# Optimization experiments

Hardware: AMD Instinct MI355X
Metric: run time of the kernel (lower is better)

## Reference

```python
import jax, jax.numpy as jnp
import numpy as np

HEADS, DHEAD = 8, 32
INNER = HEADS * DHEAD  # 256


def _conv3x3(x, w, b):
    y = jax.lax.conv_general_dilated(x, w, (1, 1), ((1, 1), (1, 1)),
                                     dimension_numbers=('NCHW', 'OIHW', 'NCHW'))
    return y + b[None, :, None, None]


def _conv1x1(x, w, b):
    return jnp.einsum('oc,bchw->bohw', w, x) + b[None, :, None, None]


def setup_inputs() -> dict:
    key = jax.random.key(0)
    ks = jax.random.split(key, 16)
    s = 0.02
    return {
        'x': jax.random.normal(ks[0], (2, 256, 48, 48), jnp.float32),
        'luma': jax.random.uniform(ks[1], (2, 1, 48, 48), jnp.float32),
        'w_qkv': jax.random.normal(ks[2], (768, 256), jnp.float32) * s,
        'b_qkv': jax.random.normal(ks[3], (768,), jnp.float32) * s,
        'w_proj': jax.random.normal(ks[4], (256, 256), jnp.float32) * s,
        'b_proj': jax.random.normal(ks[5], (256,), jnp.float32) * s,
        'w_c1': jax.random.normal(ks[6], (128, 1, 3, 3), jnp.float32) * s,
        'b_c1': jax.random.normal(ks[7], (128,), jnp.float32) * s,
        'w_c2': jax.random.normal(ks[8], (128, 128, 3, 3), jnp.float32) * s,
        'b_c2': jax.random.normal(ks[9], (128,), jnp.float32) * s,
        'w_g': jax.random.normal(ks[10], (256, 128), jnp.float32) * s,
        'b_g': jax.random.normal(ks[11], (256,), jnp.float32) * s,
        'w_bt': jax.random.normal(ks[12], (256, 128), jnp.float32) * s,
        'b_bt': jax.random.normal(ks[13], (256,), jnp.float32) * s,
        'alpha': jax.random.normal(ks[14], (), jnp.float32) * 0.1,
    }


def reference(x, luma, w_qkv, b_qkv, w_proj, b_proj, w_c1, b_c1, w_c2, b_c2,
              w_g, b_g, w_bt, b_bt, alpha):
    B, C, H, W = x.shape
    N = H * W
    scale = DHEAD ** -0.5

    def to_heads(t):  # [B, h*d, H, W] -> [B, h, N, d]
        return t.reshape(B, HEADS, DHEAD, N).transpose(0, 1, 3, 2)

    qkv = _conv1x1(x, w_qkv, b_qkv)
    q = to_heads(qkv[:, 0 * INNER:1 * INNER])
    k = to_heads(qkv[:, 1 * INNER:2 * INNER])
    v = to_heads(qkv[:, 2 * INNER:3 * INNER])

    # luma conditioning net
    h = jax.nn.relu(_conv3x3(luma, w_c1, b_c1))
    h = jax.nn.relu(_conv3x3(h, w_c2, b_c2))
    gamma = to_heads(_conv1x1(h, w_g, b_g))
    beta = to_heads(_conv1x1(h, w_bt, b_bt))
    q = gamma * q + beta
    k = gamma * k + beta
    v = gamma * v + beta

    # luminance bias: avg_pool2d(3, stride=1, pad=1, count_include_pad=True)
    invL = 1.0 - luma
    invL = jax.lax.reduce_window(invL, 0.0, jax.lax.add, (1, 1, 3, 3), (1, 1, 1, 1),
                                 ((0, 0), (0, 0), (1, 1), (1, 1))) / 9.0
    invL = invL.reshape(B, N)
    invL = invL - invL.mean(axis=-1, keepdims=True)
    q = q + alpha * invL[:, None, :, None]

    attn = jax.nn.softmax(jnp.einsum('bhid,bhjd->bhij', q, k) * scale, axis=-1)
    out = jnp.einsum('bhij,bhjd->bhid', attn, v)
    out = out.transpose(0, 1, 3, 2).reshape(B, INNER, H, W)
    return _conv1x1(out, w_proj, b_proj)
```

## Files before the change

kernel.cpp:

```cpp
#include <hip/hip_runtime.h>
#include <hip/hip_bf16.h>
#include <math.h>
#include <string.h>

#define NB 2
#define NN 2304
#define NHEADS 8
#define DH 32
#define AW 8
#define KPW 288

typedef __attribute__((ext_vector_type(8))) short v8s;
typedef __attribute__((ext_vector_type(4))) float v4f;

__device__ inline unsigned short f2b(float f) {
    unsigned u = __builtin_bit_cast(unsigned, f);
    unsigned r = u + 0x7FFFu + ((u >> 16) & 1u);
    return (unsigned short)(r >> 16);
}
__device__ inline float b2f(short s) {
    unsigned u = ((unsigned)(unsigned short)s) << 16;
    return __builtin_bit_cast(float, u);
}
__device__ inline unsigned pk2(float a, float b) {
    __hip_bfloat162 h = __float22bfloat162_rn(make_float2(a, b));
    unsigned r;
    memcpy(&r, &h, sizeof(r));
    return r;
}
__device__ inline float blo(unsigned u) { return __builtin_bit_cast(float, u << 16); }
__device__ inline float bhi(unsigned u) { return __builtin_bit_cast(float, u & 0xffff0000u); }

__global__ void k_front(const float* __restrict__ x, short* __restrict__ xt,
                        const float* __restrict__ luma, float* __restrict__ invl,
                        const float* __restrict__ wc1, const float* __restrict__ bc1,
                        short* __restrict__ h1p,
                        const float* __restrict__ wc2, const float* __restrict__ wqkv,
                        const float* __restrict__ wg, const float* __restrict__ wbt,
                        const float* __restrict__ wproj,
                        short* __restrict__ tc2b, short* __restrict__ wqkvb,
                        short* __restrict__ wgb, short* __restrict__ wbtb,
                        short* __restrict__ wprojb, float* __restrict__ vsum) {
    __shared__ unsigned short lds[64 * 66];
    __shared__ float red[256];
    int blk = blockIdx.x;
    const int XT_END = NB * 144;
    const int INVL_END = XT_END + NB;
    const int CONV1_END = INVL_END + NB * 1250;
    if (blk >= CONV1_END) {
        int i = (blk - CONV1_END) * 256 + threadIdx.x;
        if (i < 16 * DH) vsum[i] = 0.f;
        if (i < 9 * 128 * 128) {
            int s = i / (128 * 128);
            int rem = i % (128 * 128);
            int o = rem / 128, ic = rem % 128;
            tc2b[i] = (short)f2b(wc2[(o * 128 + ic) * 9 + s]);
        }
        if (i < 768 * 256) wqkvb[i] = (short)f2b(wqkv[i]);
        if (i < 256 * 128) { wgb[i] = (short)f2b(wg[i]); wbtb[i] = (short)f2b(wbt[i]); }
        if (i < 256 * 256) wprojb[i] = (short)f2b(wproj[i]);
        return;
    }
    if (blk >= INVL_END) {
        int cb = blk - INVL_END;
        int c = threadIdx.x & 127;
        int p = (cb % 1250) * 2 + (threadIdx.x >> 7);
        int b = cb / 1250;
        int py = p / 50, px = p % 50;
        float val = 0.f;
        if (py >= 1 && py <= 48 && px >= 1 && px <= 48) {
            int y = py - 1, xx0 = px - 1;
            const float* lb = luma + b * NN;
            float acc = bc1[c];
#pragma unroll
            for (int ky = 0; ky < 3; ++ky) {
                int yy = y + ky - 1;
                if (yy < 0 || yy >= 48) continue;
#pragma unroll
                for (int kx = 0; kx < 3; ++kx) {
                    int xx = xx0 + kx - 1;
                    if (xx < 0 || xx >= 48) continue;
                    acc += wc1[c * 9 + ky * 3 + kx] * lb[yy * 48 + xx];
                }
            }
            val = fmaxf(acc, 0.f);
        }
        h1p[((size_t)b * 2500 + p) * 128 + c] = (short)f2b(val);
        return;
    }
    if (blk >= XT_END) {
        int b = blk - XT_END;
        const float* lb = luma + b * NN;
        float pooled[9];
        float local = 0.f;
#pragma unroll
        for (int it = 0; it < 9; ++it) {
            int n = it * 256 + threadIdx.x;
            int y = n / 48, xx0 = n % 48;
            float s = 0.f;
            for (int ky = 0; ky < 3; ++ky) {
                int yy = y + ky - 1;
                if (yy < 0 || yy >= 48) continue;
                for (int kx = 0; kx < 3; ++kx) {
                    int xx = xx0 + kx - 1;
                    if (xx < 0 || xx >= 48) continue;
                    s += 1.f - lb[yy * 48 + xx];
                }
            }
            s *= (1.f / 9.f);
            pooled[it] = s;
            local += s;
        }
        red[threadIdx.x] = local;
        __syncthreads();
        for (int off = 128; off > 0; off >>= 1) {
            if (threadIdx.x < off) red[threadIdx.x] += red[threadIdx.x + off];
            __syncthreads();
        }
        float mean = red[0] * (1.f / NN);
#pragma unroll
        for (int it = 0; it < 9; ++it) {
            int n = it * 256 + threadIdx.x;
            invl[b * NN + n] = pooled[it] - mean;
        }
        return;
    }
    int nt = blk % 36, ct = (blk / 36) % 4, b = blk / 144;
    int n0 = nt * 64, c0 = ct * 64;
    int nc = threadIdx.x & 63, cr = threadIdx.x >> 6;
#pragma unroll
    for (int i = 0; i < 16; ++i) {
        int cs = i * 4 + cr;
        float v = x[((size_t)b * 256 + c0 + cs) * NN + n0 + nc];
        lds[nc * 66 + cs] = f2b(v);
    }
    __syncthreads();
    int cc = threadIdx.x & 31, nr = threadIdx.x >> 5;
    unsigned* xt2 = (unsigned*)xt;
#pragma unroll
    for (int j = 0; j < 8; ++j) {
        int ns = j * 8 + nr;
        unsigned w = *(unsigned*)&lds[ns * 66 + 2 * cc];
        xt2[(((size_t)b * NN + n0 + ns) * 256 + c0) / 2 + cc] = w;
    }
}

__global__ __launch_bounds__(64) void k_conv2m(const short* __restrict__ h1p,
                                               const short* __restrict__ tc2b,
                                               const float* __restrict__ bc2,
                                               short* __restrict__ h2t) {
    int lane = threadIdx.x, l15 = lane & 15, g = lane >> 4;
    int blk = blockIdx.x;
    int ntg = blk % 36, ot = (blk / 36) % 8, b = blk / (36 * 8);
    int p0[4], na[4];
#pragma unroll
    for (int j = 0; j < 4; ++j) {
        int nt = ntg * 4 + j;
        int y = nt / 3, xx = (nt % 3) * 16;
        p0[j] = (y + 1) * 50 + xx + 1;
        na[j] = y * 48 + xx + l15;
    }
    const short* hb = h1p + (size_t)b * 2500 * 128;

    v4f acc[4] = {{0.f,0.f,0.f,0.f},{0.f,0.f,0.f,0.f},{0.f,0.f,0.f,0.f},{0.f,0.f,0.f,0.f}};
#pragma unroll
    for (int s = 0; s < 9; ++s) {
        int dp = (s / 3 - 1) * 50 + (s % 3 - 1);
#pragma unroll
        for (int kk = 0; kk < 4; ++kk) {
            v8s A = *(const v8s*)(tc2b + ((size_t)(s * 128 + ot * 16 + l15)) * 128 + kk * 32 + 8 * g);
#pragma unroll
            for (int j = 0; j < 4; ++j) {
                v8s B = *(const v8s*)(hb + (size_t)(p0[j] + dp + l15) * 128 + kk * 32 + 8 * g);
                acc[j] = __builtin_amdgcn_mfma_f32_16x16x32_bf16(A, B, acc[j], 0, 0, 0);
            }
        }
    }
    v4f bias = *(const v4f*)&bc2[ot * 16 + 4 * g];
#pragma unroll
    for (int j = 0; j < 4; ++j) {
        uint2 w;
        w.x = pk2(fmaxf(acc[j][0] + bias[0], 0.f), fmaxf(acc[j][1] + bias[1], 0.f));
        w.y = pk2(fmaxf(acc[j][2] + bias[2], 0.f), fmaxf(acc[j][3] + bias[3], 0.f));
        *(uint2*)&h2t[((size_t)b * NN + na[j]) * 128 + ot * 16 + 4 * g] = w;
    }
}

__global__ __launch_bounds__(64) void k_gbm(const short* __restrict__ h2t,
                                            const short* __restrict__ wgb,
                                            const short* __restrict__ wbtb,
                                            const float* __restrict__ bg,
                                            const float* __restrict__ bbt,
                                            short* __restrict__ gtb, short* __restrict__ bttb) {
    int lane = threadIdx.x, l15 = lane & 15, g = lane >> 4;
    int blk = blockIdx.x;
    int ntg = blk % 36, ot = (blk / 36) % 16, b = blk / (36 * 16);
    int n0 = ntg * 64;
    const short* hb = h2t + (size_t)b * NN * 128;

    v4f ga[4] = {{0.f,0.f,0.f,0.f},{0.f,0.f,0.f,0.f},{0.f,0.f,0.f,0.f},{0.f,0.f,0.f,0.f}};
    v4f ta[4] = {{0.f,0.f,0.f,0.f},{0.f,0.f,0.f,0.f},{0.f,0.f,0.f,0.f},{0.f,0.f,0.f,0.f}};
#pragma unroll
    for (int kk = 0; kk < 4; ++kk) {
        v8s Ag = *(const v8s*)(wgb + (size_t)(ot * 16 + l15) * 128 + kk * 32 + 8 * g);
        v8s At = *(const v8s*)(wbtb + (size_t)(ot * 16 + l15) * 128 + kk * 32 + 8 * g);
#pragma unroll
        for (int j = 0; j < 4; ++j) {
            v8s B = *(const v8s*)(hb + (size_t)(n0 + j * 16 + l15) * 128 + kk * 32 + 8 * g);
            ga[j] = __builtin_amdgcn_mfma_f32_16x16x32_bf16(Ag, B, ga[j], 0, 0, 0);
            ta[j] = __builtin_amdgcn_mfma_f32_16x16x32_bf16(At, B, ta[j], 0, 0, 0);
        }
    }
    v4f bgv = *(const v4f*)&bg[ot * 16 + 4 * g];
    v4f bbv = *(const v4f*)&bbt[ot * 16 + 4 * g];
#pragma unroll
    for (int j = 0; j < 4; ++j) {
        size_t o = ((size_t)b * NN + n0 + j * 16 + l15) * 256 + ot * 16 + 4 * g;
        uint2 w;
        w.x = pk2(ga[j][0] + bgv[0], ga[j][1] + bgv[1]);
        w.y = pk2(ga[j][2] + bgv[2], ga[j][3] + bgv[3]);
        *(uint2*)&gtb[o] = w;
        w.x = pk2(ta[j][0] + bbv[0], ta[j][1] + bbv[1]);
        w.y = pk2(ta[j][2] + bbv[2], ta[j][3] + bbv[3]);
        *(uint2*)&bttb[o] = w;
    }
}

__global__ __launch_bounds__(64) void k_qkvm(const short* __restrict__ xt,
                                             const short* __restrict__ wqkvb,
                                             const float* __restrict__ bqkv,
                                             const short* __restrict__ gtb,
                                             const short* __restrict__ bttb,
                                             const float* __restrict__ invl,
                                             const float* __restrict__ alpha_p,
                                             short* __restrict__ qb, short* __restrict__ kb,
                                             short* __restrict__ vtb, float* __restrict__ vsum) {
    __shared__ unsigned short vlds[64][36];
    int lane = threadIdx.x, l15 = lane & 15, g = lane >> 4;
    int blk = blockIdx.x;
    int ntg = blk % 36, otg = (blk / 36) % 24, b = blk / (36 * 24);
    int n0 = ntg * 64;
    const short* xb = xt + (size_t)b * NN * 256;

    v4f acc[2][4];
#pragma unroll
    for (int oa = 0; oa < 2; ++oa)
#pragma unroll
        for (int j = 0; j < 4; ++j) acc[oa][j] = (v4f){0.f, 0.f, 0.f, 0.f};
#pragma unroll
    for (int kk = 0; kk < 8; ++kk) {
        v8s A0 = *(const v8s*)(wqkvb + (size_t)(otg * 32 + l15) * 256 + kk * 32 + 8 * g);
        v8s A1 = *(const v8s*)(wqkvb + (size_t)(otg * 32 + 16 + l15) * 256 + kk * 32 + 8 * g);
#pragma unroll
        for (int j = 0; j < 4; ++j) {
            v8s B = *(const v8s*)(xb + (size_t)(n0 + j * 16 + l15) * 256 + kk * 32 + 8 * g);
            acc[0][j] = __builtin_amdgcn_mfma_f32_16x16x32_bf16(A0, B, acc[0][j], 0, 0, 0);
            acc[1][j] = __builtin_amdgcn_mfma_f32_16x16x32_bf16(A1, B, acc[1][j], 0, 0, 0);
        }
    }
    const float scale = 0.25503486f;
    float alpha = *alpha_p;
    int which = (otg * 32) >> 8;
#pragma unroll
    for (int oa = 0; oa < 2; ++oa) {
        int ocb = otg * 32 + oa * 16;
        int cbase = (ocb & 255) + 4 * g;
        int h = cbase >> 5, dbase = cbase & 31;
        v4f bias = *(const v4f*)&bqkv[ocb + 4 * g];
        short* dst = (which == 0) ? qb : kb;
#pragma unroll
        for (int j = 0; j < 4; ++j) {
            int n = n0 + j * 16 + l15;
            v4f a = acc[oa][j];
            uint2 gg = *(const uint2*)&gtb[((size_t)b * NN + n) * 256 + cbase];
            uint2 tt = *(const uint2*)&bttb[((size_t)b * NN + n) * 256 + cbase];
            float iv = (which == 0) ? alpha * invl[b * NN + n] : 0.f;
            float v0 = blo(gg.x) * (a[0] + bias[0]) + blo(tt.x);
            float v1 = bhi(gg.x) * (a[1] + bias[1]) + bhi(tt.x);
            float v2 = blo(gg.y) * (a[2] + bias[2]) + blo(tt.y);
            float v3 = bhi(gg.y) * (a[3] + bias[3]) + bhi(tt.y);
            if (which == 0) {
                v0 = (v0 + iv) * scale; v1 = (v1 + iv) * scale;
                v2 = (v2 + iv) * scale; v3 = (v3 + iv) * scale;
            }
            uint2 wv;
            wv.x = pk2(v0, v1);
            wv.y = pk2(v2, v3);
            if (which == 2) {
                *(uint2*)&vlds[j * 16 + l15][oa * 16 + 4 * g] = wv;
            } else {
                *(uint2*)&dst[(((size_t)b * NHEADS + h) * NN + n) * DH + dbase] = wv;
            }
        }
    }
    if (which == 2) {
        __syncthreads();
        int bh = b * NHEADS + (otg - 16);
        int kb0 = ntg * 2;
        int kp = lane & 31, dh = lane >> 5;
        unsigned* vtb2 = (unsigned*)vtb;
#pragma unroll
        for (int dd = 0; dd < 16; ++dd) {
            int d = dh * 16 + dd;
            unsigned lo = vlds[2 * kp][d];
            unsigned hi = vlds[2 * kp + 1][d];
            vtb2[(((size_t)bh * 72 + kb0 + (kp >> 4)) * 32 + d) * 16 + (kp & 15)] = lo | (hi << 16);
        }
        if (lane < 32) {
            int d = lane;
            float s = 0.f;
            for (int ns = 0; ns < 64; ++ns) s += b2f((short)vlds[ns][d]);
            atomicAdd(&vsum[bh * DH + d], s);
        }
    }
}

__global__ __launch_bounds__(512) void k_attn2(const short* __restrict__ qb,
                                               const short* __restrict__ kbuf,
                                               const short* __restrict__ vtb,
                                               const float* __restrict__ vsum,
                                               short* __restrict__ aotb) {
    __shared__ short plds[AW][64 * 40];
    __shared__ short acch[AW][64][36];
    __shared__ float ps_lds[AW][64];
    int tid = threadIdx.x;
    int w = tid >> 6, lane = tid & 63;
    int l15 = lane & 15, g = lane >> 4;
    int blk = blockIdx.x;
    int logical = (blk & 7) * 72 + (blk >> 3);
    int qt = logical % 36, bh = logical / 36;
    int qbase = qt * 64;

    const short* qp = qb + ((size_t)bh * NN + qbase) * DH;
    const short* kp = kbuf + ((size_t)bh * NN + w * KPW) * DH;
    const short* vp = vtb + ((size_t)bh * 72 + w * (KPW / 32)) * 1024;

    v8s q0 = *(const v8s*)(qp + l15 * DH + 8 * g);
    v8s q1 = *(const v8s*)(qp + (16 + l15) * DH + 8 * g);
    v8s q2 = *(const v8s*)(qp + (32 + l15) * DH + 8 * g);
    v8s q3 = *(const v8s*)(qp + (48 + l15) * DH + 8 * g);

    const short one_b = (short)0x3F80;
    const v8s ones = {one_b, one_b, one_b, one_b, one_b, one_b, one_b, one_b};

    v4f acc[2][4];
#pragma unroll
    for (int dt = 0; dt < 2; ++dt)
#pragma unroll
        for (int qf = 0; qf < 4; ++qf) acc[dt][qf] = (v4f){0.f, 0.f, 0.f, 0.f};
    v4f ps[4] = {{0.f,0.f,0.f,0.f},{0.f,0.f,0.f,0.f},{0.f,0.f,0.f,0.f},{0.f,0.f,0.f,0.f}};
    short* pw = plds[w];

    for (int it = 0; it < KPW / 32; ++it) {
        const short* kpi = kp + it * 32 * DH;
        v8s ka0 = *(const v8s*)(kpi + l15 * DH + 8 * g);
        v8s ka1 = *(const v8s*)(kpi + (16 + l15) * DH + 8 * g);
        v4f s00 = __builtin_amdgcn_mfma_f32_16x16x32_bf16(ka0, q0, (v4f){0.f,0.f,0.f,0.f}, 0, 0, 0);
        v4f s01 = __builtin_amdgcn_mfma_f32_16x16x32_bf16(ka0, q1, (v4f){0.f,0.f,0.f,0.f}, 0, 0, 0);
        v4f s02 = __builtin_amdgcn_mfma_f32_16x16x32_bf16(ka0, q2, (v4f){0.f,0.f,0.f,0.f}, 0, 0, 0);
        v4f s03 = __builtin_amdgcn_mfma_f32_16x16x32_bf16(ka0, q3, (v4f){0.f,0.f,0.f,0.f}, 0, 0, 0);
        v4f s10 = __builtin_amdgcn_mfma_f32_16x16x32_bf16(ka1, q0, (v4f){0.f,0.f,0.f,0.f}, 0, 0, 0);
        v4f s11 = __builtin_amdgcn_mfma_f32_16x16x32_bf16(ka1, q1, (v4f){0.f,0.f,0.f,0.f}, 0, 0, 0);
        v4f s12 = __builtin_amdgcn_mfma_f32_16x16x32_bf16(ka1, q2, (v4f){0.f,0.f,0.f,0.f}, 0, 0, 0);
        v4f s13 = __builtin_amdgcn_mfma_f32_16x16x32_bf16(ka1, q3, (v4f){0.f,0.f,0.f,0.f}, 0, 0, 0);

#define DOFRAG(S, QF, KT)                                                        \
        {                                                                        \
            float p0 = __builtin_amdgcn_exp2f((S)[0]) - 1.f;                     \
            float p1 = __builtin_amdgcn_exp2f((S)[1]) - 1.f;                     \
            float p2 = __builtin_amdgcn_exp2f((S)[2]) - 1.f;                     \
            float p3 = __builtin_amdgcn_exp2f((S)[3]) - 1.f;                     \
            uint2 wv;                                                            \
            wv.x = pk2(p0, p1);                                                  \
            wv.y = pk2(p2, p3);                                                  \
            *(uint2*)((char*)pw + ((QF) * 16 + l15) * 80 + ((KT) * 16 + 4 * g) * 2) = wv; \
        }
        DOFRAG(s00, 0, 0)
        DOFRAG(s01, 1, 0)
        DOFRAG(s02, 2, 0)
        DOFRAG(s03, 3, 0)
        DOFRAG(s10, 0, 1)
        DOFRAG(s11, 1, 1)
        DOFRAG(s12, 2, 1)
        DOFRAG(s13, 3, 1)
#undef DOFRAG
        v8s pa0 = *(v8s*)((char*)pw + l15 * 80 + 16 * g);
        v8s pa1 = *(v8s*)((char*)pw + (16 + l15) * 80 + 16 * g);
        v8s pa2 = *(v8s*)((char*)pw + (32 + l15) * 80 + 16 * g);
        v8s pa3 = *(v8s*)((char*)pw + (48 + l15) * 80 + 16 * g);
        const short* vpi = vp + it * 1024;
        v8s vb0 = *(const v8s*)(vpi + l15 * 32 + 8 * g);
        v8s vb1 = *(const v8s*)(vpi + (16 + l15) * 32 + 8 * g);
        __builtin_amdgcn_s_setprio(1);
        acc[0][0] = __builtin_amdgcn_mfma_f32_16x16x32_bf16(pa0, vb0, acc[0][0], 0, 0, 0);
        acc[1][0] = __builtin_amdgcn_mfma_f32_16x16x32_bf16(pa0, vb1, acc[1][0], 0, 0, 0);
        acc[0][1] = __builtin_amdgcn_mfma_f32_16x16x32_bf16(pa1, vb0, acc[0][1], 0, 0, 0);
        acc[1][1] = __builtin_amdgcn_mfma_f32_16x16x32_bf16(pa1, vb1, acc[1][1], 0, 0, 0);
        acc[0][2] = __builtin_amdgcn_mfma_f32_16x16x32_bf16(pa2, vb0, acc[0][2], 0, 0, 0);
        acc[1][2] = __builtin_amdgcn_mfma_f32_16x16x32_bf16(pa2, vb1, acc[1][2], 0, 0, 0);
        acc[0][3] = __builtin_amdgcn_mfma_f32_16x16x32_bf16(pa3, vb0, acc[0][3], 0, 0, 0);
        acc[1][3] = __builtin_amdgcn_mfma_f32_16x16x32_bf16(pa3, vb1, acc[1][3], 0, 0, 0);
        ps[0] = __builtin_amdgcn_mfma_f32_16x16x32_bf16(pa0, ones, ps[0], 0, 0, 0);
        ps[1] = __builtin_amdgcn_mfma_f32_16x16x32_bf16(pa1, ones, ps[1], 0, 0, 0);
        ps[2] = __builtin_amdgcn_mfma_f32_16x16x32_bf16(pa2, ones, ps[2], 0, 0, 0);
        ps[3] = __builtin_amdgcn_mfma_f32_16x16x32_bf16(pa3, ones, ps[3], 0, 0, 0);
        __builtin_amdgcn_s_setprio(0);
    }

    if (l15 == 0) {
#pragma unroll
        for (int qf = 0; qf < 4; ++qf)
#pragma unroll
            for (int r = 0; r < 4; ++r)
                ps_lds[w][qf * 16 + 4 * g + r] = ps[qf][r];
    }
#pragma unroll
    for (int qf = 0; qf < 4; ++qf)
#pragma unroll
        for (int r = 0; r < 4; ++r) {
            acch[w][qf * 16 + 4 * g + r][l15]      = (short)f2b(acc[0][qf][r]);
            acch[w][qf * 16 + 4 * g + r][16 + l15] = (short)f2b(acc[1][qf][r]);
        }
    __syncthreads();

    int q = tid >> 3, d0 = (tid & 7) * 4;
    float L = (float)NN;
    float a0 = 0.f, a1 = 0.f, a2 = 0.f, a3 = 0.f;
#pragma unroll
    for (int wv = 0; wv < AW; ++wv) {
        L += ps_lds[wv][q];
        const short* row = &acch[wv][q][d0];
        a0 += b2f(row[0]); a1 += b2f(row[1]); a2 += b2f(row[2]); a3 += b2f(row[3]);
    }
    const float* vs = vsum + bh * DH + d0;
    float rl = 1.f / L;
    uint2 o;
    o.x = pk2((a0 + vs[0]) * rl, (a1 + vs[1]) * rl);
    o.y = pk2((a2 + vs[2]) * rl, (a3 + vs[3]) * rl);
    int b = bh >> 3, h = bh & 7;
    *(uint2*)&aotb[((size_t)b * NN + qbase + q) * 256 + h * DH + d0] = o;
}

__global__ __launch_bounds__(64) void k_projm(const short* __restrict__ aotb,
                                              const short* __restrict__ wprojb,
                                              const float* __restrict__ bproj,
                                              float* __restrict__ out) {
    int lane = threadIdx.x, l15 = lane & 15, g = lane >> 4;
    int blk = blockIdx.x;
    int ntg = blk % 36, otg = (blk / 36) % 8, b = blk / (36 * 8);
    int n0 = ntg * 64;
    const short* ab = aotb + (size_t)b * NN * 256;

    v4f acc[2][4];
#pragma unroll
    for (int oa = 0; oa < 2; ++oa)
#pragma unroll
        for (int j = 0; j < 4; ++j) acc[oa][j] = (v4f){0.f, 0.f, 0.f, 0.f};
#pragma unroll
    for (int kk = 0; kk < 8; ++kk) {
        v8s A0 = *(const v8s*)(wprojb + (size_t)(otg * 32 + l15) * 256 + kk * 32 + 8 * g);
        v8s A1 = *(const v8s*)(wprojb + (size_t)(otg * 32 + 16 + l15) * 256 + kk * 32 + 8 * g);
#pragma unroll
        for (int j = 0; j < 4; ++j) {
            v8s B = *(const v8s*)(ab + (size_t)(n0 + j * 16 + l15) * 256 + kk * 32 + 8 * g);
            acc[0][j] = __builtin_amdgcn_mfma_f32_16x16x32_bf16(A0, B, acc[0][j], 0, 0, 0);
            acc[1][j] = __builtin_amdgcn_mfma_f32_16x16x32_bf16(A1, B, acc[1][j], 0, 0, 0);
        }
    }
#pragma unroll
    for (int oa = 0; oa < 2; ++oa) {
        v4f bias = *(const v4f*)&bproj[otg * 32 + oa * 16 + 4 * g];
#pragma unroll
        for (int j = 0; j < 4; ++j) {
#pragma unroll
            for (int r = 0; r < 4; ++r) {
                int o = otg * 32 + oa * 16 + 4 * g + r;
                out[((size_t)b * 256 + o) * NN + n0 + j * 16 + l15] = acc[oa][j][r] + bias[r];
            }
        }
    }
}

extern "C" void kernel_launch(void* const* d_in, const int* in_sizes, int n_in,
                              void* d_out, int out_size, void* d_ws, size_t ws_size,
                              hipStream_t stream) {
    const float* x     = (const float*)d_in[0];
    const float* luma  = (const float*)d_in[1];
    const float* wqkv  = (const float*)d_in[2];
    const float* bqkv  = (const float*)d_in[3];
    const float* wproj = (const float*)d_in[4];
    const float* bproj = (const float*)d_in[5];
    const float* wc1   = (const float*)d_in[6];
    const float* bc1   = (const float*)d_in[7];
    const float* wc2   = (const float*)d_in[8];
    const float* bc2   = (const float*)d_in[9];
    const float* wg    = (const float*)d_in[10];
    const float* bg    = (const float*)d_in[11];
    const float* wbt   = (const float*)d_in[12];
    const float* bbt   = (const float*)d_in[13];
    const float* alpha = (const float*)d_in[14];
    float* out = (float*)d_out;

    float* ws = (float*)d_ws;
    size_t off = 0;
    short* tc2b = (short*)(ws + off);  off += 9 * 128 * 128 / 2;
    short* wqkvb = (short*)(ws + off); off += 768 * 256 / 2;
    short* wgb = (short*)(ws + off);   off += 256 * 128 / 2;
    short* wbtb = (short*)(ws + off);  off += 256 * 128 / 2;
    short* wprojb = (short*)(ws + off); off += 256 * 256 / 2;
    short* h1p = (short*)(ws + off);   off += NB * 2500 * 128 / 2;
    short* xt = (short*)(ws + off);    off += NB * NN * 256 / 2;
    short* h2t = (short*)(ws + off);   off += NB * NN * 128 / 2;
    short* gtb = (short*)(ws + off);   off += NB * NN * 256 / 2;
    short* bttb = (short*)(ws + off);  off += NB * NN * 256 / 2;
    float* invl = ws + off;            off += NB * NN;
    short* qbb = (short*)(ws + off);   off += 16 * NN * DH / 2;
    short* kbb = (short*)(ws + off);   off += 16 * NN * DH / 2;
    short* vtb = (short*)(ws + off);   off += 16 * NN * DH / 2;
    float* vsum = ws + off;            off += 16 * DH;
    short* aotb = (short*)(ws + off);  off += NB * NN * 256 / 2;
    (void)ws_size; (void)in_sizes; (void)n_in; (void)out_size;

    int front_grid = NB * 144 + NB + NB * 1250 + 768;
    k_front<<<front_grid, 256, 0, stream>>>(x, xt, luma, invl, wc1, bc1, h1p,
                                            wc2, wqkv, wg, wbt, wproj,
                                            tc2b, wqkvb, wgb, wbtb, wprojb, vsum);
    k_conv2m<<<NB * 8 * 36, 64, 0, stream>>>(h1p, tc2b, bc2, h2t);
    k_gbm<<<NB * 16 * 36, 64, 0, stream>>>(h2t, wgb, wbtb, bg, bbt, gtb, bttb);
    k_qkvm<<<NB * 24 * 36, 64, 0, stream>>>(xt, wqkvb, bqkv, gtb, bttb, invl, alpha,
                                            qbb, kbb, vtb, vsum);
    k_attn2<<<576, 512, 0, stream>>>(qbb, kbb, vtb, vsum, aotb);
    k_projm<<<NB * 8 * 36, 64, 0, stream>>>(aotb, wprojb, bproj, out);
}
```

Baseline: 96.11 us.

## Use 32x32x16 MFMA in attention with register-resident P and smaller query tiles

Switches the attention kernel from 16x16x32 to 32x32x16 bf16 MFMA. K rows are loaded in a permuted order so the score accumulator layout already matches the A-operand layout for the PV product. This drops the per-iteration LDS round trip for the probability tile. The query tile shrinks from 64 to 32, which doubles the grid to 1152 blocks and halves the per-wave work, while each block still repeats the K/V loads.

```diff
diff --git a/kernel.cpp b/kernel.cpp
--- a/kernel.cpp
+++ b/kernel.cpp
@@ -12,6 +12,7 @@
 
 typedef __attribute__((ext_vector_type(8))) short v8s;
 typedef __attribute__((ext_vector_type(4))) float v4f;
+typedef __attribute__((ext_vector_type(16))) float v16f;
 
 __device__ inline unsigned short f2b(float f) {
     unsigned u = __builtin_bit_cast(unsigned, f);
@@ -320,125 +321,92 @@
                                                const short* __restrict__ vtb,
                                                const float* __restrict__ vsum,
                                                short* __restrict__ aotb) {
-    __shared__ short plds[AW][64 * 40];
-    __shared__ short acch[AW][64][36];
-    __shared__ float ps_lds[AW][64];
+    __shared__ short acch[AW][32][33];
+    __shared__ float ps_lds[AW][32];
     int tid = threadIdx.x;
     int w = tid >> 6, lane = tid & 63;
-    int l15 = lane & 15, g = lane >> 4;
+    int l31 = lane & 31, h = lane >> 5;
     int blk = blockIdx.x;
-    int logical = (blk & 7) * 72 + (blk >> 3);
-    int qt = logical % 36, bh = logical / 36;
-    int qbase = qt * 64;
+    int logical = (blk & 7) * 144 + (blk >> 3);
+    int qt = logical % 72, bh = logical / 72;
+    int qbase = qt * 32;
 
     const short* qp = qb + ((size_t)bh * NN + qbase) * DH;
     const short* kp = kbuf + ((size_t)bh * NN + w * KPW) * DH;
     const short* vp = vtb + ((size_t)bh * 72 + w * (KPW / 32)) * 1024;
 
-    v8s q0 = *(const v8s*)(qp + l15 * DH + 8 * g);
-    v8s q1 = *(const v8s*)(qp + (16 + l15) * DH + 8 * g);
-    v8s q2 = *(const v8s*)(qp + (32 + l15) * DH + 8 * g);
-    v8s q3 = *(const v8s*)(qp + (48 + l15) * DH + 8 * g);
+    int m = l31;
+    int sig = 16 * (m >> 4) + 8 * ((m >> 2) & 1) + 4 * ((m >> 3) & 1) + (m & 3);
+
+    v8s q0 = *(const v8s*)(qp + l31 * DH + 8 * h);
+    v8s q1 = *(const v8s*)(qp + l31 * DH + 16 + 8 * h);
 
     const short one_b = (short)0x3F80;
     const v8s ones = {one_b, one_b, one_b, one_b, one_b, one_b, one_b, one_b};
-
-    v4f acc[2][4];
-#pragma unroll
-    for (int dt = 0; dt < 2; ++dt)
-#pragma unroll
-        for (int qf = 0; qf < 4; ++qf) acc[dt][qf] = (v4f){0.f, 0.f, 0.f, 0.f};
-    v4f ps[4] = {{0.f,0.f,0.f,0.f},{0.f,0.f,0.f,0.f},{0.f,0.f,0.f,0.f},{0.f,0.f,0.f,0.f}};
-    short* pw = plds[w];
+    const v16f vz = {0.f,0.f,0.f,0.f,0.f,0.f,0.f,0.f,0.f,0.f,0.f,0.f,0.f,0.f,0.f,0.f};
+
+    v16f accO = vz, ps = vz;
 
     for (int it = 0; it < KPW / 32; ++it) {
         const short* kpi = kp + it * 32 * DH;
-        v8s ka0 = *(const v8s*)(kpi + l15 * DH + 8 * g);
-        v8s ka1 = *(const v8s*)(kpi + (16 + l15) * DH + 8 * g);
-        v4f s00 = __builtin_amdgcn_mfma_f32_16x16x32_bf16(ka0, q0, (v4f){0.f,0.f,0.f,0.f}, 0, 0, 0);
-        v4f s01 = __builtin_amdgcn_mfma_f32_16x16x32_bf16(ka0, q1, (v4f){0.f,0.f,0.f,0.f}, 0, 0, 0);
-        v4f s02 = __builtin_amdgcn_mfma_f32_16x16x32_bf16(ka0, q2, (v4f){0.f,0.f,0.f,0.f}, 0, 0, 0);
-        v4f s03 = __builtin_amdgcn_mfma_f32_16x16x32_bf16(ka0, q3, (v4f){0.f,0.f,0.f,0.f}, 0, 0, 0);
-        v4f s10 = __builtin_amdgcn_mfma_f32_16x16x32_bf16(ka1, q0, (v4f){0.f,0.f,0.f,0.f}, 0, 0, 0);
-        v4f s11 = __builtin_amdgcn_mfma_f32_16x16x32_bf16(ka1, q1, (v4f){0.f,0.f,0.f,0.f}, 0, 0, 0);
-        v4f s12 = __builtin_amdgcn_mfma_f32_16x16x32_bf16(ka1, q2, (v4f){0.f,0.f,0.f,0.f}, 0, 0, 0);
-        v4f s13 = __builtin_amdgcn_mfma_f32_16x16x32_bf16(ka1, q3, (v4f){0.f,0.f,0.f,0.f}, 0, 0, 0);
-
-#define DOFRAG(S, QF, KT)                                                        \
-        {                                                                        \
-            float p0 = __builtin_amdgcn_exp2f((S)[0]) - 1.f;                     \
-            float p1 = __builtin_amdgcn_exp2f((S)[1]) - 1.f;                     \
-            float p2 = __builtin_amdgcn_exp2f((S)[2]) - 1.f;                     \
-            float p3 = __builtin_amdgcn_exp2f((S)[3]) - 1.f;                     \
-            uint2 wv;                                                            \
-            wv.x = pk2(p0, p1);                                                  \
-            wv.y = pk2(p2, p3);                                                  \
-            *(uint2*)((char*)pw + ((QF) * 16 + l15) * 80 + ((KT) * 16 + 4 * g) * 2) = wv; \
-        }
-        DOFRAG(s00, 0, 0)
-        DOFRAG(s01, 1, 0)
-        DOFRAG(s02, 2, 0)
-        DOFRAG(s03, 3, 0)
-        DOFRAG(s10, 0, 1)
-        DOFRAG(s11, 1, 1)
-        DOFRAG(s12, 2, 1)
-        DOFRAG(s13, 3, 1)
-#undef DOFRAG
-        v8s pa0 = *(v8s*)((char*)pw + l15 * 80 + 16 * g);
-        v8s pa1 = *(v8s*)((char*)pw + (16 + l15) * 80 + 16 * g);
-        v8s pa2 = *(v8s*)((char*)pw + (32 + l15) * 80 + 16 * g);
-        v8s pa3 = *(v8s*)((char*)pw + (48 + l15) * 80 + 16 * g);
+        v8s ka0 = *(const v8s*)(kpi + sig * DH + 8 * h);
+        v8s ka1 = *(const v8s*)(kpi + sig * DH + 16 + 8 * h);
+        v16f sC = __builtin_amdgcn_mfma_f32_32x32x16_bf16(ka0, q0, vz, 0, 0, 0);
+        sC = __builtin_amdgcn_mfma_f32_32x32x16_bf16(ka1, q1, sC, 0, 0, 0);
+
+        float p[16];
+#pragma unroll
+        for (int r = 0; r < 16; ++r) p[r] = __builtin_amdgcn_exp2f(sC[r]) - 1.f;
+        unsigned w0[4], w1[4];
+#pragma unroll
+        for (int i = 0; i < 4; ++i) {
+            w0[i] = pk2(p[2 * i], p[2 * i + 1]);
+            w1[i] = pk2(p[8 + 2 * i], p[9 + 2 * i]);
+        }
+        v8s pa0, pa1;
+        memcpy(&pa0, w0, 16);
+        memcpy(&pa1, w1, 16);
+
         const short* vpi = vp + it * 1024;
-        v8s vb0 = *(const v8s*)(vpi + l15 * 32 + 8 * g);
-        v8s vb1 = *(const v8s*)(vpi + (16 + l15) * 32 + 8 * g);
+        v8s vb0 = *(const v8s*)(vpi + l31 * 32 + 8 * h);
+        v8s vb1 = *(const v8s*)(vpi + l31 * 32 + 16 + 8 * h);
+
         __builtin_amdgcn_s_setprio(1);
-        acc[0][0] = __builtin_amdgcn_mfma_f32_16x16x32_bf16(pa0, vb0, acc[0][0], 0, 0, 0);
-        acc[1][0] = __builtin_amdgcn_mfma_f32_16x16x32_bf16(pa0, vb1, acc[1][0], 0, 0, 0);
-        acc[0][1] = __builtin_amdgcn_mfma_f32_16x16x32_bf16(pa1, vb0, acc[0][1], 0, 0, 0);
-        acc[1][1] = __builtin_amdgcn_mfma_f32_16x16x32_bf16(pa1, vb1, acc[1][1], 0, 0, 0);
-        acc[0][2] = __builtin_amdgcn_mfma_f32_16x16x32_bf16(pa2, vb0, acc[0][2], 0, 0, 0);
-        acc[1][2] = __builtin_amdgcn_mfma_f32_16x16x32_bf16(pa2, vb1, acc[1][2], 0, 0, 0);
-        acc[0][3] = __builtin_amdgcn_mfma_f32_16x16x32_bf16(pa3, vb0, acc[0][3], 0, 0, 0);
-        acc[1][3] = __builtin_amdgcn_mfma_f32_16x16x32_bf16(pa3, vb1, acc[1][3], 0, 0, 0);
-        ps[0] = __builtin_amdgcn_mfma_f32_16x16x32_bf16(pa0, ones, ps[0], 0, 0, 0);
-        ps[1] = __builtin_amdgcn_mfma_f32_16x16x32_bf16(pa1, ones, ps[1], 0, 0, 0);
-        ps[2] = __builtin_amdgcn_mfma_f32_16x16x32_bf16(pa2, ones, ps[2], 0, 0, 0);
-        ps[3] = __builtin_amdgcn_mfma_f32_16x16x32_bf16(pa3, ones, ps[3], 0, 0, 0);
+        accO = __builtin_amdgcn_mfma_f32_32x32x16_bf16(pa0, vb0, accO, 0, 0, 0);
+        accO = __builtin_amdgcn_mfma_f32_32x32x16_bf16(pa1, vb1, accO, 0, 0, 0);
+        ps = __builtin_amdgcn_mfma_f32_32x32x16_bf16(pa0, ones, ps, 0, 0, 0);
+        ps = __builtin_amdgcn_mfma_f32_32x32x16_bf16(pa1, ones, ps, 0, 0, 0);
         __builtin_amdgcn_s_setprio(0);
     }
 
-    if (l15 == 0) {
-#pragma unroll
-        for (int qf = 0; qf < 4; ++qf)
-#pragma unroll
-            for (int r = 0; r < 4; ++r)
-                ps_lds[w][qf * 16 + 4 * g + r] = ps[qf][r];
-    }
-#pragma unroll
-    for (int qf = 0; qf < 4; ++qf)
-#pragma unroll
-        for (int r = 0; r < 4; ++r) {
-            acch[w][qf * 16 + 4 * g + r][l15]      = (short)f2b(acc[0][qf][r]);
-            acch[w][qf * 16 + 4 * g + r][16 + l15] = (short)f2b(acc[1][qf][r]);
-        }
+#pragma unroll
+    for (int r = 0; r < 16; ++r) {
+        int qr = (r & 3) + 8 * (r >> 2) + 4 * h;
+        acch[w][qr][l31] = (short)f2b(accO[r]);
+    }
+    if (l31 == 0) {
+#pragma unroll
+        for (int r = 0; r < 16; ++r) {
+            int qr = (r & 3) + 8 * (r >> 2) + 4 * h;
+            ps_lds[w][qr] = ps[r];
+        }
+    }
     __syncthreads();
 
-    int q = tid >> 3, d0 = (tid & 7) * 4;
+    int q = tid >> 4, d0 = (tid & 15) * 2;
     float L = (float)NN;
-    float a0 = 0.f, a1 = 0.f, a2 = 0.f, a3 = 0.f;
+    float a0 = 0.f, a1 = 0.f;
 #pragma unroll
     for (int wv = 0; wv < AW; ++wv) {
         L += ps_lds[wv][q];
-        const short* row = &acch[wv][q][d0];
-        a0 += b2f(row[0]); a1 += b2f(row[1]); a2 += b2f(row[2]); a3 += b2f(row[3]);
+        a0 += b2f(acch[wv][q][d0]);
+        a1 += b2f(acch[wv][q][d0 + 1]);
     }
     const float* vs = vsum + bh * DH + d0;
     float rl = 1.f / L;
-    uint2 o;
-    o.x = pk2((a0 + vs[0]) * rl, (a1 + vs[1]) * rl);
-    o.y = pk2((a2 + vs[2]) * rl, (a3 + vs[3]) * rl);
-    int b = bh >> 3, h = bh & 7;
-    *(uint2*)&aotb[((size_t)b * NN + qbase + q) * 256 + h * DH + d0] = o;
+    unsigned o = pk2((a0 + vs[0]) * rl, (a1 + vs[1]) * rl);
+    int b = bh >> 3, hh = bh & 7;
+    *(unsigned*)&aotb[((size_t)b * NN + qbase + q) * 256 + hh * DH + d0] = o;
 }
 
 __global__ __launch_bounds__(64) void k_projm(const short* __restrict__ aotb,
@@ -529,6 +497,6 @@
     k_gbm<<<NB * 16 * 36, 64, 0, stream>>>(h2t, wgb, wbtb, bg, bbt, gtb, bttb);
     k_qkvm<<<NB * 24 * 36, 64, 0, stream>>>(xt, wqkvb, bqkv, gtb, bttb, invl, alpha,
                                             qbb, kbb, vtb, vsum);
-    k_attn2<<<576, 512, 0, stream>>>(qbb, kbb, vtb, vsum, aotb);
+    k_attn2<<<1152, 512, 0, stream>>>(qbb, kbb, vtb, vsum, aotb);
     k_projm<<<NB * 8 * 36, 64, 0, stream>>>(aotb, wprojb, bproj, out);
 }
```

Result: faster. 91.67 us (median of 2 runs) (-4.6%).
